# Kernel optimization log

Hardware: AMD Instinct MI355X
Metric: run time of the kernel (lower is better)

Reference implementation:

```python
import jax, jax.numpy as jnp
import numpy as np

B, T, D = 4, 2048, 2048
H = 16
HD = D // H  # head_dim = 128


def setup_inputs() -> dict:
    key = jax.random.key(0)
    ks = jax.random.split(key, 10)
    s = 0.02
    return {
        "x": jax.random.normal(ks[0], (B, T, D), dtype=jnp.float32),
        "Wq": jax.random.normal(ks[1], (D, D), dtype=jnp.float32) * s,
        "bq": jnp.zeros((D,), dtype=jnp.float32),
        "Wk": jax.random.normal(ks[2], (D, D), dtype=jnp.float32) * s,
        "bk": jnp.zeros((D,), dtype=jnp.float32),
        "Wv": jax.random.normal(ks[3], (D, D), dtype=jnp.float32) * s,
        "bv": jnp.zeros((D,), dtype=jnp.float32),
        "Wo": jax.random.normal(ks[4], (D, D), dtype=jnp.float32) * s,
        "bo": jnp.zeros((D,), dtype=jnp.float32),
    }


def reference(x, Wq, bq, Wk, bk, Wv, bv, Wo, bo):
    b, t, _ = x.shape
    # projections (nn.Linear: x @ W.T + b); split heads -> (b, h, t, hd)
    def split_heads(y):
        return y.reshape(b, t, H, HD).transpose(0, 2, 1, 3)

    q = split_heads(x @ Wq.T + bq)
    k = split_heads(x @ Wk.T + bk)
    v = split_heads(x @ Wv.T + bv)

    scale = 1.0 / jnp.sqrt(jnp.float32(HD))
    scores = jnp.einsum("bhqd,bhkd->bhqk", q, k) * scale  # (b,h,t,t)
    causal = jnp.triu(jnp.ones((t, t), dtype=bool), k=1)
    scores = jnp.where(causal, -jnp.inf, scores)
    attn = jax.nn.softmax(scores, axis=-1)
    # dropout p=0.0 -> identity
    ctx = jnp.einsum("bhqk,bhkd->bhqd", attn, v)  # (b,h,t,hd)
    ctx = ctx.transpose(0, 2, 1, 3).reshape(b, t, D)
    return ctx @ Wo.T + bo
```

## Files before the change

### kernel.cpp

```cpp
#include <hip/hip_runtime.h>
#include <hip/hip_bf16.h>

typedef __attribute__((ext_vector_type(8))) __bf16 bf16x8;
typedef __attribute__((ext_vector_type(4))) __bf16 bf16x4;
typedef __attribute__((ext_vector_type(4))) short s16x4;
typedef __attribute__((ext_vector_type(4))) float f32x4;
typedef unsigned int u32;

#define LOG2E 1.4426950408889634f

__device__ __forceinline__ void gload_lds16(const void* g, void* l) {
  __builtin_amdgcn_global_load_lds(
      (const __attribute__((address_space(1))) u32*)g,
      (__attribute__((address_space(3))) u32*)l, 16, 0, 0);
}

__global__ __launch_bounds__(256)
void cvt_f32_bf16(const float* __restrict__ src, __hip_bfloat16* __restrict__ dst, int n4) {
  int i = blockIdx.x * blockDim.x + threadIdx.x;
  if (i < n4) {
    float4 v = ((const float4*)src)[i];
    union { unsigned long long u; __hip_bfloat16 h[4]; } o;
    o.h[0] = __float2bfloat16(v.x);
    o.h[1] = __float2bfloat16(v.y);
    o.h[2] = __float2bfloat16(v.z);
    o.h[3] = __float2bfloat16(v.w);
    ((unsigned long long*)dst)[i] = o.u;
  }
}

__global__ __launch_bounds__(256)
void cvt_all(const float* __restrict__ x,
             const float* __restrict__ w0, const float* __restrict__ w1,
             const float* __restrict__ w2, const float* __restrict__ w3,
             __hip_bfloat16* __restrict__ xb,
             __hip_bfloat16* __restrict__ b0, __hip_bfloat16* __restrict__ b1,
             __hip_bfloat16* __restrict__ b2, __hip_bfloat16* __restrict__ b3,
             int n4x, int n4wlog)
{
  int i = blockIdx.x * blockDim.x + threadIdx.x;
  const float* src; __hip_bfloat16* dst; int off;
  if (i < n4x) { src = x; dst = xb; off = i; }
  else {
    int j = i - n4x;
    int which = j >> n4wlog;
    off = j & ((1 << n4wlog) - 1);
    src = which == 0 ? w0 : which == 1 ? w1 : which == 2 ? w2 : w3;
    dst = which == 0 ? b0 : which == 1 ? b1 : which == 2 ? b2 : b3;
  }
  float4 v = ((const float4*)src)[off];
  union { unsigned long long u; __hip_bfloat16 h[4]; } o;
  o.h[0] = __float2bfloat16(v.x);
  o.h[1] = __float2bfloat16(v.y);
  o.h[2] = __float2bfloat16(v.z);
  o.h[3] = __float2bfloat16(v.w);
  ((unsigned long long*)dst)[off] = o.u;
}

template<int MODE>
__global__ __launch_bounds__(256, 2)
void gemm_bt(const __hip_bfloat16* __restrict__ A,
             const __hip_bfloat16* __restrict__ W,
             const float* __restrict__ bias,
             __hip_bfloat16* __restrict__ C,
             float* __restrict__ Cf,
             int M, int N, int K, float oscale)
{
  constexpr int BM = 128, BN = 128, BK = 64;
  __shared__ __align__(16) __hip_bfloat16 As[BM * BK];
  __shared__ __align__(16) __hip_bfloat16 Bs[BN * BK];

  const int tid = threadIdx.x;
  const int lane = tid & 63;
  const int w = tid >> 6;
  const int wr = w >> 1, wc = w & 1;
  const int quad = lane >> 4, l15 = lane & 15;
  const int m0 = blockIdx.x * BM;
  const int n0 = blockIdx.y * BN;

  f32x4 acc[4][4] = {};

  int offs[4], rows[4], kbs[4];
  for (int i = 0; i < 4; ++i) {
    int off = (tid + i * 256) * 16;
    int row = off >> 7;
    int cpos = (off >> 4) & 7;
    int csrc = cpos ^ (row & 7);
    offs[i] = off; rows[i] = row; kbs[i] = csrc * 8;
  }

  for (int k0 = 0; k0 < K; k0 += BK) {
    for (int i = 0; i < 4; ++i)
      gload_lds16(A + (size_t)(m0 + rows[i]) * K + k0 + kbs[i], (char*)As + offs[i]);
    for (int i = 0; i < 4; ++i)
      gload_lds16(W + (size_t)(n0 + rows[i]) * K + k0 + kbs[i], (char*)Bs + offs[i]);
    __syncthreads();

    for (int ks = 0; ks < 2; ++ks) {
      bf16x8 af[4], bfr[4];
      for (int i = 0; i < 4; ++i) {
        int row = wr * 64 + i * 16 + l15;
        int ph = (ks * 4 + quad) ^ (row & 7);
        af[i] = *(const bf16x8*)((const char*)As + row * 128 + ph * 16);
      }
      for (int j = 0; j < 4; ++j) {
        int row = wc * 64 + j * 16 + l15;
        int ph = (ks * 4 + quad) ^ (row & 7);
        bfr[j] = *(const bf16x8*)((const char*)Bs + row * 128 + ph * 16);
      }
      for (int i = 0; i < 4; ++i)
        for (int j = 0; j < 4; ++j)
          acc[i][j] = __builtin_amdgcn_mfma_f32_16x16x32_bf16(af[i], bfr[j], acc[i][j], 0, 0, 0);
    }
    __syncthreads();
  }

  for (int i = 0; i < 4; ++i) {
    int mbase = m0 + wr * 64 + i * 16 + quad * 4;
    for (int j = 0; j < 4; ++j) {
      int n = n0 + wc * 64 + j * 16 + l15;
      float bv = bias[n];
      for (int r = 0; r < 4; ++r) {
        int m = mbase + r;
        float v = (acc[i][j][r] + bv) * oscale;
        if (MODE == 0) {
          C[(size_t)m * N + n] = __float2bfloat16(v);
        } else if (MODE == 1) {
          int b = m >> 11, t = m & 2047;
          C[((size_t)(b * 2048 + n)) * 2048 + t] = __float2bfloat16(v);
        } else {
          Cf[(size_t)m * N + n] = v;
        }
      }
    }
  }
}

__global__ __launch_bounds__(256, 2)
void attn_fwd(const __hip_bfloat16* __restrict__ Q,
              const __hip_bfloat16* __restrict__ K,
              const __hip_bfloat16* __restrict__ Vt,
              __hip_bfloat16* __restrict__ ctx)
{
  __shared__ __align__(16) __hip_bfloat16 KVl[2][16384];

  const int tid = threadIdx.x;
  const int lane = tid & 63;
  const int w = tid >> 6;
  const int quad = lane >> 4, l15 = lane & 15;
  const int bid = blockIdx.x;
  const int qi = 15 - (bid >> 6);
  const int bh = bid & 63;
  const int b = bh >> 4, h = bh & 15;
  const int q0 = qi * 128;

  bf16x8 qf[2][4];
  for (int sub = 0; sub < 2; ++sub) {
    const __hip_bfloat16* qp =
        Q + ((size_t)(b * 2048 + q0 + sub * 64 + w * 16 + l15)) * 2048 + h * 128 + quad * 8;
    for (int ks = 0; ks < 4; ++ks) qf[sub][ks] = *(const bf16x8*)(qp + ks * 32);
  }

  int krow[4], kcol[4], vrow[4], vcol[4], soff[4];
  for (int p = 0; p < 4; ++p) {
    int off = (tid + p * 256) * 16;
    soff[p] = off;
    int r1 = off >> 8;
    int pc1 = (off >> 4) & 15;
    krow[p] = r1; kcol[p] = ((pc1 & 8) | ((pc1 & 7) ^ (r1 & 7))) * 8;
    int r2 = off >> 7;
    int pc2 = (off >> 4) & 7;
    vrow[p] = r2; vcol[p] = (pc2 ^ (r2 & 7)) * 8;
  }

  f32x4 o[2][8] = {};
  float lsum[2] = {0.f, 0.f};
  const int base0 = q0 + w * 16;
  const int base1 = q0 + 64 + w * 16;

  const int ktmax = (q0 + 127) >> 6;

  for (int p = 0; p < 4; ++p)
    gload_lds16(K + ((size_t)(b * 2048 + krow[p])) * 2048 + h * 128 + kcol[p],
                (char*)&KVl[0][0] + soff[p]);
  for (int p = 0; p < 4; ++p)
    gload_lds16(Vt + ((size_t)(b * 2048 + h * 128 + vrow[p])) * 2048 + vcol[p],
                (char*)&KVl[0][8192] + soff[p]);
  __syncthreads();

  for (int kt = 0; kt <= ktmax; ++kt) {
    const int cur = kt & 1;
    const int kbase = kt * 64;
    if (kt < ktmax) {
      const int nbase = kbase + 64;
      for (int p = 0; p < 4; ++p)
        gload_lds16(K + ((size_t)(b * 2048 + nbase + krow[p])) * 2048 + h * 128 + kcol[p],
                    (char*)&KVl[1 - cur][0] + soff[p]);
      for (int p = 0; p < 4; ++p)
        gload_lds16(Vt + ((size_t)(b * 2048 + h * 128 + vrow[p])) * 2048 + nbase + vcol[p],
                    (char*)&KVl[1 - cur][8192] + soff[p]);
    }

    const char* Kl = (const char*)&KVl[cur][0];
    const char* Vl = (const char*)&KVl[cur][8192];

    const bool act0 = kbase <= base0 + 15;
    const bool act1 = kbase <= base1 + 15;

    f32x4 s[2][4] = {};
    for (int ct = 0; ct < 4; ++ct) {
      int row = ct * 16 + l15;
      for (int ks = 0; ks < 4; ++ks) {
        int c = ks * 4 + quad;
        int ph = (c & 8) | ((c & 7) ^ (row & 7));
        bf16x8 kf = *(const bf16x8*)(Kl + row * 256 + ph * 16);
        if (act0) s[0][ct] = __builtin_amdgcn_mfma_f32_16x16x32_bf16(kf, qf[0][ks], s[0][ct], 0, 0, 0);
        if (act1) s[1][ct] = __builtin_amdgcn_mfma_f32_16x16x32_bf16(kf, qf[1][ks], s[1][ct], 0, 0, 0);
      }
    }

    s16x4 pf[2][4];
    for (int sub = 0; sub < 2; ++sub) {
      if (!(sub ? act1 : act0)) continue;
      const int bs = sub ? base1 : base0;
      const bool full = (kbase + 63 <= bs);
      float lsv = lsum[sub];
      for (int ct = 0; ct < 4; ++ct) {
        bf16x4 pb;
        if (full) {
          for (int r = 0; r < 4; ++r) {
            float e = exp2f(s[sub][ct][r]);
            lsv += e; pb[r] = (__bf16)e;
          }
        } else {
          int diff = (bs + l15) - (kbase + ct * 16 + quad * 4);
          for (int r = 0; r < 4; ++r) {
            float e = (r <= diff) ? exp2f(s[sub][ct][r]) : 0.f;
            lsv += e; pb[r] = (__bf16)e;
          }
        }
        pf[sub][ct] = __builtin_bit_cast(s16x4, pb);
      }
      lsum[sub] = lsv;
    }

    for (int dgrp = 0; dgrp < 8; ++dgrp) {
      int row = dgrp * 16 + l15;
      for (int ct = 0; ct < 4; ++ct) {
        int c = ct * 2 + (quad >> 1);
        int ph = c ^ (row & 7);
        s16x4 vf = *(const s16x4*)(Vl + row * 128 + ph * 16 + (quad & 1) * 8);
        if (act0) o[0][dgrp] = __builtin_amdgcn_mfma_f32_16x16x16bf16_1k(vf, pf[0][ct], o[0][dgrp], 0, 0, 0);
        if (act1) o[1][dgrp] = __builtin_amdgcn_mfma_f32_16x16x16bf16_1k(vf, pf[1][ct], o[1][dgrp], 0, 0, 0);
      }
    }
    __syncthreads();
  }

  for (int sub = 0; sub < 2; ++sub) {
    float ls = lsum[sub];
    ls += __shfl_xor(ls, 16, 64);
    ls += __shfl_xor(ls, 32, 64);
    lsum[sub] = 1.0f / ls;
  }

  for (int sub = 0; sub < 2; ++sub) {
    char* rb = (char*)&KVl[0][0] + (w * 2 + sub) * 4096;
    float inv = lsum[sub];
    for (int dgrp = 0; dgrp < 8; ++dgrp) {
      for (int rp = 0; rp < 2; ++rp) {
        __hip_bfloat16 lo = __float2bfloat16(o[sub][dgrp][rp * 2] * inv);
        __hip_bfloat16 hi = __float2bfloat16(o[sub][dgrp][rp * 2 + 1] * inv);
        u32 pk = (u32)*(unsigned short*)&lo | ((u32)*(unsigned short*)&hi << 16);
        int c = dgrp * 2 + (quad >> 1);
        int cp = c ^ (l15 & 7);
        *(u32*)(rb + l15 * 256 + cp * 16 + (quad & 1) * 8 + rp * 4) = pk;
      }
    }
    int q2 = lane & 15;
    int qq = q0 + sub * 64 + w * 16 + q2;
    __hip_bfloat16* cp = ctx + ((size_t)(b * 2048 + qq)) * 2048 + h * 128;
    for (int rr = 0; rr < 4; ++rr) {
      int cl = quad + rr * 4;
      int cph = cl ^ (q2 & 7);
      uint4 val = *(const uint4*)(rb + q2 * 256 + cph * 16);
      *(uint4*)(cp + cl * 8) = val;
    }
  }
}

extern "C" void kernel_launch(void* const* d_in, const int* in_sizes, int n_in,
                              void* d_out, int out_size, void* d_ws, size_t ws_size,
                              hipStream_t stream)
{
  (void)in_sizes; (void)n_in; (void)out_size;
  const float* x  = (const float*)d_in[0];
  const float* Wq = (const float*)d_in[1];
  const float* bq = (const float*)d_in[2];
  const float* Wk = (const float*)d_in[3];
  const float* bk = (const float*)d_in[4];
  const float* Wv = (const float*)d_in[5];
  const float* bv = (const float*)d_in[6];
  const float* Wo = (const float*)d_in[7];
  const float* bo = (const float*)d_in[8];
  float* out = (float*)d_out;

  const int M = 8192, D = 2048;
  const size_t MD = (size_t)M * D, DD = (size_t)D * D;
  const int n4x = (int)(MD / 4), n4w = (int)(DD / 4);
  dim3 cb(256), gg(64, 16), bb(256), ga(1024);
  const float qscale = 0.08838834764831845f * LOG2E;

  if (ws_size >= (4 * MD + 4 * DD) * 2) {
    __hip_bfloat16* xb  = (__hip_bfloat16*)d_ws;
    __hip_bfloat16* Wqb = xb  + MD;
    __hip_bfloat16* Wkb = Wqb + DD;
    __hip_bfloat16* Wvb = Wkb + DD;
    __hip_bfloat16* Wob = Wvb + DD;
    __hip_bfloat16* Qb  = Wob + DD;
    __hip_bfloat16* Kb  = Qb  + MD;
    __hip_bfloat16* Vtb = Kb  + MD;
    __hip_bfloat16* Cx  = xb;

    int tot4 = n4x + 4 * n4w;
    hipLaunchKernelGGL(cvt_all, dim3(tot4 / 256), cb, 0, stream,
                       x, Wq, Wk, Wv, Wo, xb, Wqb, Wkb, Wvb, Wob, n4x, 20);
    hipLaunchKernelGGL((gemm_bt<0>), gg, bb, 0, stream, xb, Wqb, bq, Qb, (float*)nullptr, M, D, D, qscale);
    hipLaunchKernelGGL((gemm_bt<0>), gg, bb, 0, stream, xb, Wkb, bk, Kb, (float*)nullptr, M, D, D, 1.0f);
    hipLaunchKernelGGL((gemm_bt<1>), gg, bb, 0, stream, xb, Wvb, bv, Vtb, (float*)nullptr, M, D, D, 1.0f);
    hipLaunchKernelGGL(attn_fwd, ga, bb, 0, stream, Qb, Kb, Vtb, Cx);
    hipLaunchKernelGGL((gemm_bt<2>), gg, bb, 0, stream, Cx, Wob, bo, (__hip_bfloat16*)nullptr, out, M, D, D, 1.0f);
  } else {
    __hip_bfloat16* xb  = (__hip_bfloat16*)d_ws;
    __hip_bfloat16* Wb  = xb  + MD;
    __hip_bfloat16* Qb  = Wb  + DD;
    __hip_bfloat16* Kb  = Qb  + MD;
    __hip_bfloat16* Vtb = Kb  + MD;
    __hip_bfloat16* Cx  = xb;

    dim3 cgx((n4x + 255) / 256), cgw((n4w + 255) / 256);
    hipLaunchKernelGGL(cvt_f32_bf16, cgx, cb, 0, stream, x, xb, n4x);
    hipLaunchKernelGGL(cvt_f32_bf16, cgw, cb, 0, stream, Wq, Wb, n4w);
    hipLaunchKernelGGL((gemm_bt<0>), gg, bb, 0, stream, xb, Wb, bq, Qb, (float*)nullptr, M, D, D, qscale);
    hipLaunchKernelGGL(cvt_f32_bf16, cgw, cb, 0, stream, Wk, Wb, n4w);
    hipLaunchKernelGGL((gemm_bt<0>), gg, bb, 0, stream, xb, Wb, bk, Kb, (float*)nullptr, M, D, D, 1.0f);
    hipLaunchKernelGGL(cvt_f32_bf16, cgw, cb, 0, stream, Wv, Wb, n4w);
    hipLaunchKernelGGL((gemm_bt<1>), gg, bb, 0, stream, xb, Wb, bv, Vtb, (float*)nullptr, M, D, D, 1.0f);
    hipLaunchKernelGGL(attn_fwd, ga, bb, 0, stream, Qb, Kb, Vtb, Cx);
    hipLaunchKernelGGL(cvt_f32_bf16, cgw, cb, 0, stream, Wo, Wb, n4w);
    hipLaunchKernelGGL((gemm_bt<2>), gg, bb, 0, stream, Cx, Wb, bo, (__hip_bfloat16*)nullptr, out, M, D, D, 1.0f);
  }
}
```

Before: 568.4 us.

## Replace GEMM with 256x256 double-buffered, phase-pipelined 8-wave kernel

Replaces the 128x128 single-buffered GEMM with a 256x256 tile kernel using 512 threads, double-buffered LDS, and four compute phases per K-step. Each phase interleaves global-to-LDS loads for the next tile with MFMA work, using explicit waitcnt/barrier control and s_setprio, plus an L2-friendly block swizzle. The goal is to raise data reuse and hide memory latency in the four projection GEMMs. In exchange it needs 128KB of LDS per block and many accumulator registers, which may limit occupancy.

```diff
diff --git a/kernel.cpp b/kernel.cpp
--- a/kernel.cpp
+++ b/kernel.cpp
@@ -57,79 +57,139 @@
   ((unsigned long long*)dst)[off] = o.u;
 }
 
+#define VMW(N) asm volatile("s_waitcnt vmcnt(" #N ")" ::: "memory")
+
+#define GPHASE(P, MH, NH, RDA, RDB, ISSUE, WAITC, LGHINT)                      \
+  {                                                                            \
+    if (RDA) {                                                                 \
+      _Pragma("unroll")                                                        \
+      for (int i = 0; i < 4; ++i) {                                            \
+        const char* pa = Ab + (((MH) * 128 + wr * 64 + i * 16 + l15) << 7);    \
+        afr[i][0] = *(const bf16x8*)(pa + ph0);                                \
+        afr[i][1] = *(const bf16x8*)(pa + ph1);                                \
+      }                                                                        \
+    }                                                                          \
+    if (RDB) {                                                                 \
+      _Pragma("unroll")                                                        \
+      for (int j = 0; j < 2; ++j) {                                            \
+        const char* pb = Bb + (((NH) * 128 + wc * 32 + j * 16 + l15) << 7);    \
+        bfr[j][0] = *(const bf16x8*)(pb + ph0);                                \
+        bfr[j][1] = *(const bf16x8*)(pb + ph1);                                \
+      }                                                                        \
+    }                                                                          \
+    ISSUE;                                                                     \
+    WAITC;                                                                     \
+    LGHINT;                                                                    \
+    __builtin_amdgcn_s_barrier();                                              \
+    asm volatile("s_waitcnt lgkmcnt(0)" ::: "memory");                         \
+    __builtin_amdgcn_sched_barrier(0);                                         \
+    __builtin_amdgcn_s_setprio(1);                                             \
+    _Pragma("unroll")                                                          \
+    for (int ks = 0; ks < 2; ++ks)                                             \
+      _Pragma("unroll")                                                        \
+      for (int i = 0; i < 4; ++i)                                              \
+        _Pragma("unroll")                                                      \
+        for (int j = 0; j < 2; ++j)                                            \
+          acc[P][i][j] = __builtin_amdgcn_mfma_f32_16x16x32_bf16(              \
+              afr[i][ks], bfr[j][ks], acc[P][i][j], 0, 0, 0);                  \
+    __builtin_amdgcn_s_setprio(0);                                             \
+    __builtin_amdgcn_s_barrier();                                              \
+  }
+
 template<int MODE>
-__global__ __launch_bounds__(256, 2)
-void gemm_bt(const __hip_bfloat16* __restrict__ A,
+__global__ __launch_bounds__(512, 2)
+void gemm256(const __hip_bfloat16* __restrict__ A,
              const __hip_bfloat16* __restrict__ W,
              const float* __restrict__ bias,
              __hip_bfloat16* __restrict__ C,
              float* __restrict__ Cf,
              int M, int N, int K, float oscale)
 {
-  constexpr int BM = 128, BN = 128, BK = 64;
-  __shared__ __align__(16) __hip_bfloat16 As[BM * BK];
-  __shared__ __align__(16) __hip_bfloat16 Bs[BN * BK];
+  __shared__ __align__(16) __hip_bfloat16 SH[2][32768];
 
   const int tid = threadIdx.x;
   const int lane = tid & 63;
   const int w = tid >> 6;
-  const int wr = w >> 1, wc = w & 1;
+  const int wr = w >> 2, wc = w & 3;
   const int quad = lane >> 4, l15 = lane & 15;
-  const int m0 = blockIdx.x * BM;
-  const int n0 = blockIdx.y * BN;
-
-  f32x4 acc[4][4] = {};
-
-  int offs[4], rows[4], kbs[4];
-  for (int i = 0; i < 4; ++i) {
-    int off = (tid + i * 256) * 16;
-    int row = off >> 7;
-    int cpos = (off >> 4) & 7;
-    int csrc = cpos ^ (row & 7);
-    offs[i] = off; rows[i] = row; kbs[i] = csrc * 8;
-  }
-
-  for (int k0 = 0; k0 < K; k0 += BK) {
-    for (int i = 0; i < 4; ++i)
-      gload_lds16(A + (size_t)(m0 + rows[i]) * K + k0 + kbs[i], (char*)As + offs[i]);
-    for (int i = 0; i < 4; ++i)
-      gload_lds16(W + (size_t)(n0 + rows[i]) * K + k0 + kbs[i], (char*)Bs + offs[i]);
-    __syncthreads();
-
-    for (int ks = 0; ks < 2; ++ks) {
-      bf16x8 af[4], bfr[4];
-      for (int i = 0; i < 4; ++i) {
-        int row = wr * 64 + i * 16 + l15;
-        int ph = (ks * 4 + quad) ^ (row & 7);
-        af[i] = *(const bf16x8*)((const char*)As + row * 128 + ph * 16);
-      }
-      for (int j = 0; j < 4; ++j) {
-        int row = wc * 64 + j * 16 + l15;
-        int ph = (ks * 4 + quad) ^ (row & 7);
-        bfr[j] = *(const bf16x8*)((const char*)Bs + row * 128 + ph * 16);
-      }
-      for (int i = 0; i < 4; ++i)
-        for (int j = 0; j < 4; ++j)
-          acc[i][j] = __builtin_amdgcn_mfma_f32_16x16x32_bf16(af[i], bfr[j], acc[i][j], 0, 0, 0);
-    }
-    __syncthreads();
-  }
-
-  for (int i = 0; i < 4; ++i) {
-    int mbase = m0 + wr * 64 + i * 16 + quad * 4;
-    for (int j = 0; j < 4; ++j) {
-      int n = n0 + wc * 64 + j * 16 + l15;
-      float bv = bias[n];
-      for (int r = 0; r < 4; ++r) {
-        int m = mbase + r;
-        float v = (acc[i][j][r] + bv) * oscale;
-        if (MODE == 0) {
-          C[(size_t)m * N + n] = __float2bfloat16(v);
-        } else if (MODE == 1) {
-          int b = m >> 11, t = m & 2047;
-          C[((size_t)(b * 2048 + n)) * 2048 + t] = __float2bfloat16(v);
-        } else {
-          Cf[(size_t)m * N + n] = v;
+
+  const int nb = N >> 8;
+  const int swz = (blockIdx.x & 7) * ((int)gridDim.x >> 3) + ((int)blockIdx.x >> 3);
+  const int m0 = (swz / nb) << 8;
+  const int n0 = (swz % nb) << 8;
+
+  const int NT = K >> 6;
+
+  const int r0 = tid >> 3;
+  const int kb = ((tid & 7) ^ (r0 & 7)) << 3;
+  const __hip_bfloat16* Ag = A + (size_t)(m0 + r0) * K + kb;
+  const __hip_bfloat16* Wg = W + (size_t)(n0 + r0) * K + kb;
+
+  const int ph0 = (quad ^ (l15 & 7)) << 4;
+  const int ph1 = ((4 + quad) ^ (l15 & 7)) << 4;
+
+  f32x4 acc[4][4][2] = {};
+  bf16x8 afr[4][2], bfr[2][2];
+
+  auto issueA = [&](int t2, int mh) {
+    if (t2 < NT) {
+      const __hip_bfloat16* g = Ag + (size_t)(mh * 128) * K + (t2 << 6);
+      char* l = (char*)SH[t2 & 1] + mh * 16384 + (tid << 4);
+      gload_lds16(g, l);
+      gload_lds16(g + (size_t)64 * K, l + 8192);
+    }
+  };
+  auto issueB = [&](int t2, int nh) {
+    if (t2 < NT) {
+      const __hip_bfloat16* g = Wg + (size_t)(nh * 128) * K + (t2 << 6);
+      char* l = (char*)SH[t2 & 1] + 32768 + nh * 16384 + (tid << 4);
+      gload_lds16(g, l);
+      gload_lds16(g + (size_t)64 * K, l + 8192);
+    }
+  };
+
+  issueA(0, 0); issueB(0, 0); issueA(0, 1); issueB(0, 1);
+  VMW(4);
+  __builtin_amdgcn_s_barrier();
+
+  for (int t = 0; t < NT; ++t) {
+    const char* Ab = (const char*)SH[t & 1];
+    const char* Bb = Ab + 32768;
+    const bool more = (t + 1 < NT);
+
+    GPHASE(0, 0, 0, true, true, issueA(t + 1, 0),
+           if (more) { VMW(4); } else { VMW(2); },
+           asm volatile("s_waitcnt lgkmcnt(8)" ::: "memory"));
+    GPHASE(1, 1, 0, true, false, issueB(t + 1, 0),
+           if (more) { VMW(4); } else { VMW(0); }, );
+    GPHASE(2, 1, 1, false, true, issueA(t + 1, 1), , );
+    GPHASE(3, 0, 1, true, false, issueB(t + 1, 1),
+           if (more) { VMW(4); }, );
+  }
+
+#pragma unroll
+  for (int p = 0; p < 4; ++p) {
+    const int mh = (p == 1 || p == 2) ? 1 : 0;
+    const int nh = (p >= 2) ? 1 : 0;
+#pragma unroll
+    for (int i = 0; i < 4; ++i) {
+      int mbase = m0 + mh * 128 + wr * 64 + i * 16 + quad * 4;
+#pragma unroll
+      for (int j = 0; j < 2; ++j) {
+        int n = n0 + nh * 128 + wc * 32 + j * 16 + l15;
+        float bv = bias[n];
+#pragma unroll
+        for (int r = 0; r < 4; ++r) {
+          int mm = mbase + r;
+          float v = (acc[p][i][j][r] + bv) * oscale;
+          if (MODE == 0) {
+            C[(size_t)mm * N + n] = __float2bfloat16(v);
+          } else if (MODE == 1) {
+            int b = mm >> 11, tt = mm & 2047;
+            C[((size_t)(b * 2048 + n)) * 2048 + tt] = __float2bfloat16(v);
+          } else {
+            Cf[(size_t)mm * N + n] = v;
+          }
         }
       }
     }
@@ -308,7 +368,8 @@
   const int M = 8192, D = 2048;
   const size_t MD = (size_t)M * D, DD = (size_t)D * D;
   const int n4x = (int)(MD / 4), n4w = (int)(DD / 4);
-  dim3 cb(256), gg(64, 16), bb(256), ga(1024);
+  dim3 cb(256), bb(256), ga(1024);
+  dim3 gg((M / 256) * (D / 256)), gbb(512);
   const float qscale = 0.08838834764831845f * LOG2E;
 
   if (ws_size >= (4 * MD + 4 * DD) * 2) {
@@ -325,11 +386,11 @@
     int tot4 = n4x + 4 * n4w;
     hipLaunchKernelGGL(cvt_all, dim3(tot4 / 256), cb, 0, stream,
                        x, Wq, Wk, Wv, Wo, xb, Wqb, Wkb, Wvb, Wob, n4x, 20);
-    hipLaunchKernelGGL((gemm_bt<0>), gg, bb, 0, stream, xb, Wqb, bq, Qb, (float*)nullptr, M, D, D, qscale);
-    hipLaunchKernelGGL((gemm_bt<0>), gg, bb, 0, stream, xb, Wkb, bk, Kb, (float*)nullptr, M, D, D, 1.0f);
-    hipLaunchKernelGGL((gemm_bt<1>), gg, bb, 0, stream, xb, Wvb, bv, Vtb, (float*)nullptr, M, D, D, 1.0f);
+    hipLaunchKernelGGL((gemm256<0>), gg, gbb, 0, stream, xb, Wqb, bq, Qb, (float*)nullptr, M, D, D, qscale);
+    hipLaunchKernelGGL((gemm256<0>), gg, gbb, 0, stream, xb, Wkb, bk, Kb, (float*)nullptr, M, D, D, 1.0f);
+    hipLaunchKernelGGL((gemm256<1>), gg, gbb, 0, stream, xb, Wvb, bv, Vtb, (float*)nullptr, M, D, D, 1.0f);
     hipLaunchKernelGGL(attn_fwd, ga, bb, 0, stream, Qb, Kb, Vtb, Cx);
-    hipLaunchKernelGGL((gemm_bt<2>), gg, bb, 0, stream, Cx, Wob, bo, (__hip_bfloat16*)nullptr, out, M, D, D, 1.0f);
+    hipLaunchKernelGGL((gemm256<2>), gg, gbb, 0, stream, Cx, Wob, bo, (__hip_bfloat16*)nullptr, out, M, D, D, 1.0f);
   } else {
     __hip_bfloat16* xb  = (__hip_bfloat16*)d_ws;
     __hip_bfloat16* Wb  = xb  + MD;
@@ -341,13 +402,13 @@
     dim3 cgx((n4x + 255) / 256), cgw((n4w + 255) / 256);
     hipLaunchKernelGGL(cvt_f32_bf16, cgx, cb, 0, stream, x, xb, n4x);
     hipLaunchKernelGGL(cvt_f32_bf16, cgw, cb, 0, stream, Wq, Wb, n4w);
-    hipLaunchKernelGGL((gemm_bt<0>), gg, bb, 0, stream, xb, Wb, bq, Qb, (float*)nullptr, M, D, D, qscale);
+    hipLaunchKernelGGL((gemm256<0>), gg, gbb, 0, stream, xb, Wb, bq, Qb, (float*)nullptr, M, D, D, qscale);
     hipLaunchKernelGGL(cvt_f32_bf16, cgw, cb, 0, stream, Wk, Wb, n4w);
-    hipLaunchKernelGGL((gemm_bt<0>), gg, bb, 0, stream, xb, Wb, bk, Kb, (float*)nullptr, M, D, D, 1.0f);
+    hipLaunchKernelGGL((gemm256<0>), gg, gbb, 0, stream, xb, Wb, bk, Kb, (float*)nullptr, M, D, D, 1.0f);
     hipLaunchKernelGGL(cvt_f32_bf16, cgw, cb, 0, stream, Wv, Wb, n4w);
-    hipLaunchKernelGGL((gemm_bt<1>), gg, bb, 0, stream, xb, Wb, bv, Vtb, (float*)nullptr, M, D, D, 1.0f);
+    hipLaunchKernelGGL((gemm256<1>), gg, gbb, 0, stream, xb, Wb, bv, Vtb, (float*)nullptr, M, D, D, 1.0f);
     hipLaunchKernelGGL(attn_fwd, ga, bb, 0, stream, Qb, Kb, Vtb, Cx);
     hipLaunchKernelGGL(cvt_f32_bf16, cgw, cb, 0, stream, Wo, Wb, n4w);
-    hipLaunchKernelGGL((gemm_bt<2>), gg, bb, 0, stream, Cx, Wb, bo, (__hip_bfloat16*)nullptr, out, M, D, D, 1.0f);
-  }
-}
+    hipLaunchKernelGGL((gemm256<2>), gg, gbb, 0, stream, Cx, Wb, bo, (__hip_bfloat16*)nullptr, out, M, D, D, 1.0f);
+  }
+}
```

Result: no change. 557.8 us (-1.8%).
